# Kernel tuning notes

Hardware: AMD Instinct MI355X
Metric: run time of the kernel (lower is better)

The kernel has to match this reference:

```python
import jax, jax.numpy as jnp
import numpy as np

WS = 4      # window_size
H = 128     # hidden_size
IN = 3      # input_size (1 control + 2 state channels)
OUT = 2     # out_size = input_size - 1


def _lstm_layer(x, Wih, Whh, b):
    # x: [B, S, Din] -> ys: [B, S, H], h/c: [B, H]. PyTorch gate order i,f,g,o.
    B = x.shape[0]
    xg = jnp.einsum('bsd,gd->bsg', x, Wih) + b  # precompute input projections

    def step(carry, xt):
        h, c = carry
        g = xt + h @ Whh.T
        i, f, gg, o = jnp.split(g, 4, axis=-1)
        c = jax.nn.sigmoid(f) * c + jax.nn.sigmoid(i) * jnp.tanh(gg)
        h = jax.nn.sigmoid(o) * jnp.tanh(c)
        return (h, c), h

    z = jnp.zeros((B, Whh.shape[1]), x.dtype)
    (h, c), ys = jax.lax.scan(step, (z, z), xg.transpose(1, 0, 2))
    return ys.transpose(1, 0, 2), h, c


def _lstm2(x, p):
    (Wih0, Whh0, b0), (Wih1, Whh1, b1) = p
    y0, h0, c0 = _lstm_layer(x, Wih0, Whh0, b0)
    y1, h1, c1 = _lstm_layer(y0, Wih1, Whh1, b1)
    return y1, jnp.stack([h0, h1]), jnp.stack([c0, c1])


def _forward(traj, Wih0, Whh0, bih0, bhh0, Wih1, Whh1, bih1, bhh1, Wl, bl):
    p = ((Wih0, Whh0, bih0 + bhh0), (Wih1, Whh1, bih1 + bhh1))
    head = lambda ys: ys[:, -1] @ Wl.T + bl  # linear applied to last LSTM step (== pred[:, -1])
    T = traj.shape[1]

    # initial window on raw trajectory
    ys, h, c = _lstm2(traj[:, :WS], p)
    out = traj[:, WS - 1:WS, 1:] + head(ys)[:, None, :]  # [B, 1, OUT]

    # warm-up phase: windows mix raw traj rows with predicted rows (features ordered [ctrl, out])
    for t in range(1, WS):
        tmp = jnp.concatenate([traj[:, WS + t:WS + t + 1, 0:1], out[:, t - 1:t, :]], axis=2)
        seq = jnp.concatenate([traj[:, t:WS + t - 1, :], tmp], axis=1)  # [B, WS, IN]
        ys, h, c = _lstm2(seq, p)
        out = jnp.concatenate([out, traj[:, WS + t - 1:WS + t, 1:] + head(ys)[:, None, :]], axis=1)

    nsteps = T - 2 * WS
    idx = WS + np.arange(nsteps)[:, None] + np.arange(WS)[None, :]  # [nsteps, WS]
    ctrl = traj[:, :, 0][:, idx].transpose(1, 0, 2)[..., None]      # [nsteps, B, WS, 1]

    def step(carry, ctrl_t):
        win, _, _ = carry
        seq = jnp.concatenate([win, ctrl_t], axis=2)  # [B, WS, OUT+1]
        ys, h, c = _lstm2(seq, p)
        new = win[:, -1, :] + head(ys)                # [B, OUT]
        win = jnp.concatenate([win[:, 1:], new[:, None, :]], axis=1)
        return (win, h, c), new

    (win, h, c), news = jax.lax.scan(step, (out, h, c), ctrl)
    out = jnp.concatenate([out, news.transpose(1, 0, 2)], axis=1)  # [B, T-WS, OUT]
    return out, h, c


def setup_inputs():
    key = jax.random.key(0)
    ks = jax.random.split(key, 11)
    B, T = 128, 256
    s = 1.0 / np.sqrt(H)
    u = lambda k, shp: jax.random.uniform(k, shp, jnp.float32, -s, s)
    return dict(
        one_full_traj=jax.random.normal(ks[0], (B, T, IN), jnp.float32),
        Wih0=u(ks[1], (4 * H, IN)), Whh0=u(ks[2], (4 * H, H)),
        bih0=u(ks[3], (4 * H,)), bhh0=u(ks[4], (4 * H,)),
        Wih1=u(ks[5], (4 * H, H)), Whh1=u(ks[6], (4 * H, H)),
        bih1=u(ks[7], (4 * H,)), bhh1=u(ks[8], (4 * H,)),
        Wl=u(ks[9], (OUT, H)), bl=u(ks[10], (OUT,)),
    )


def reference(one_full_traj, Wih0, Whh0, bih0, bhh0, Wih1, Whh1, bih1, bhh1, Wl, bl):
    # returns (out, h_n, c_n) matching torch's (out, hidden)
    return _forward(one_full_traj, Wih0, Whh0, bih0, bhh0, Wih1, Whh1, bih1, bhh1, Wl, bl)
```

## Files before the change

### kernel.cpp

```cpp
#include <hip/hip_runtime.h>

typedef _Float16 half2_t __attribute__((ext_vector_type(2)));
typedef unsigned int u32;

#define NW 252

__device__ inline u32 pk(float x, float y) {
  half2_t h; h.x = (_Float16)x; h.y = (_Float16)y;
  return __builtin_bit_cast(u32, h);
}

__device__ inline float fdot2(u32 a, u32 b, float c) {
#if __has_builtin(__builtin_amdgcn_fdot2)
  return __builtin_amdgcn_fdot2(__builtin_bit_cast(half2_t, a),
                                __builtin_bit_cast(half2_t, b), c, false);
#else
  half2_t ah = __builtin_bit_cast(half2_t, a);
  half2_t bh = __builtin_bit_cast(half2_t, b);
  return c + (float)ah.x * (float)bh.x + (float)ah.y * (float)bh.y;
#endif
}

__device__ inline float fast_rcp(float x) {
#if __has_builtin(__builtin_amdgcn_rcpf)
  return __builtin_amdgcn_rcpf(x);
#else
  return 1.0f / x;
#endif
}

__device__ inline float sigf(float x)  { return fast_rcp(1.0f + __expf(-x)); }
__device__ inline float tanh_(float x) { return 1.0f - 2.0f * fast_rcp(__expf(2.0f * x) + 1.0f); }

__device__ inline float quad_reduce(float v) {
  int x = __builtin_bit_cast(int, v);
  int y = __builtin_amdgcn_update_dpp(0, x, 0xB1, 0xF, 0xF, true);
  v += __builtin_bit_cast(float, y);
  x = __builtin_bit_cast(int, v);
  y = __builtin_amdgcn_update_dpp(0, x, 0x4E, 0xF, 0xF, true);
  v += __builtin_bit_cast(float, y);
  return v;
}

#define LOAD_SLICE(dst, basehalf)                                          \
  { const uint4* _p = (const uint4*)(basehalf) + ks * 4;                   \
    uint4 _q0 = _p[0], _q1 = _p[1], _q2 = _p[2], _q3 = _p[3];              \
    dst[0]=_q0.x;  dst[1]=_q0.y;  dst[2]=_q0.z;  dst[3]=_q0.w;             \
    dst[4]=_q1.x;  dst[5]=_q1.y;  dst[6]=_q1.z;  dst[7]=_q1.w;             \
    dst[8]=_q2.x;  dst[9]=_q2.y;  dst[10]=_q2.z; dst[11]=_q2.w;            \
    dst[12]=_q3.x; dst[13]=_q3.y; dst[14]=_q3.z; dst[15]=_q3.w; }


#define L0STEP(w_, t_, p_) {                                               \
    float x0, x1, x2;                                                      \
    if ((w_) < 4) {                                                        \
      if ((w_) == 0 || (t_) < 3) {                                         \
        const float* r_ = &trajS[((w_) + (t_)) * 3];                       \
        x0 = r_[0]; x1 = r_[1]; x2 = r_[2];                                \
      } else {                        \
        x0 = trajS[(4 + (w_)) * 3];                                        \
        x1 = preds[((w_) - 1) * 2];                                        \
        x2 = preds[((w_) - 1) * 2 + 1];                                    \
      }                                                                    \
    } else {                                       \
      const int s_ = (w_) - 4;                                             \
      x0 = preds[(s_ + (t_)) * 2];                                         \
      x1 = preds[(s_ + (t_)) * 2 + 1];                                     \
      x2 = trajS[((w_) + (t_)) * 3];                                       \
    }                                                                      \
    const bool lead_ = (ks == 0);                                          \
    float a0_ = b0r[0] + w0r[0]*x0 + w0r[1] *x1 + w0r[2] *x2;              \
    float a1_ = b0r[1] + w0r[3]*x0 + w0r[4] *x1 + w0r[5] *x2;              \
    float a2_ = b0r[2] + w0r[6]*x0 + w0r[7] *x1 + w0r[8] *x2;              \
    float a3_ = b0r[3] + w0r[9]*x0 + w0r[10]*x1 + w0r[11]*x2;              \
    float acc0 = lead_ ? a0_ : 0.f, acc1 = lead_ ? a1_ : 0.f;              \
    float acc2 = lead_ ? a2_ : 0.f, acc3 = lead_ ? a3_ : 0.f;              \
    if ((t_) > 0) {                                                        \
      u32 su[16];                                                          \
      LOAD_SLICE(su, h0buf[p_]);                                           \
      _Pragma("unroll")                                                    \
      for (int kk = 0; kk < 16; ++kk) {                                    \
        acc0 = fdot2(wA[     kk], su[kk], acc0);                           \
        acc1 = fdot2(wA[16 + kk], su[kk], acc1);                           \
        acc2 = fdot2(wA[32 + kk], su[kk], acc2);                           \
        acc3 = fdot2(wA[48 + kk], su[kk], acc3);                           \
      }                                                                    \
    }                                                                      \
    acc0 = quad_reduce(acc0); acc1 = quad_reduce(acc1);                    \
    acc2 = quad_reduce(acc2); acc3 = quad_reduce(acc3);                    \
    float ig_ = sigf(acc0), fg_ = sigf(acc1);                              \
    float gg_ = tanh_(acc2), og_ = sigf(acc3);                             \
    float cp_ = (t_) ? c0 : 0.f;                                           \
    c0  = fg_ * cp_ + ig_ * gg_;                                           \
    h0f = og_ * tanh_(c0);                                                 \
    if (lead_) h0buf[(p_) ^ 1][j] = (_Float16)h0f;                         \
  }

#define L1STEP(t_, p_) {                                                   \
    const bool lead_ = (ks == 0);                                          \
    float acc0 = lead_ ? b1r[0] : 0.f, acc1 = lead_ ? b1r[1] : 0.f;        \
    float acc2 = lead_ ? b1r[2] : 0.f, acc3 = lead_ ? b1r[3] : 0.f;        \
    {                                                                      \
      u32 sy[16];                                                          \
      LOAD_SLICE(sy, h0buf[p_]);                        \
      _Pragma("unroll")                                                    \
      for (int kk = 0; kk < 16; ++kk) {                                    \
        acc0 = fdot2(wB[     kk], sy[kk], acc0);                           \
        acc1 = fdot2(wB[16 + kk], sy[kk], acc1);                           \
        acc2 = fdot2(wB[32 + kk], sy[kk], acc2);                           \
        acc3 = fdot2(wB[48 + kk], sy[kk], acc3);                           \
      }                                                                    \
    }                                                                      \
    if ((t_) > 0) {                                                        \
      u32 sh[16];                                                          \
      LOAD_SLICE(sh, h1buf[p_]);                                           \
      _Pragma("unroll")                                                    \
      for (int kk = 0; kk < 16; ++kk) {                                    \
        acc0 = fdot2(wC[     kk], sh[kk], acc0);                           \
        acc1 = fdot2(wC[16 + kk], sh[kk], acc1);                           \
        acc2 = fdot2(wC[32 + kk], sh[kk], acc2);                           \
        acc3 = fdot2(wC[48 + kk], sh[kk], acc3);                           \
      }                                                                    \
    }                                                                      \
    acc0 = quad_reduce(acc0); acc1 = quad_reduce(acc1);                    \
    acc2 = quad_reduce(acc2); acc3 = quad_reduce(acc3);                    \
    float ig_ = sigf(acc0), fg_ = sigf(acc1);                              \
    float gg_ = tanh_(acc2), og_ = sigf(acc3);                             \
    float cp_ = (t_) ? c1 : 0.f;                                           \
    c1  = fg_ * cp_ + ig_ * gg_;                                           \
    h1f = og_ * tanh_(c1);                                                 \
    if (lead_) {                                                           \
      h1buf[(p_) ^ 1][j] = (_Float16)h1f;                                  \
      if ((t_) == 3) sh_h1f[j] = h1f;           \
    }                                                                      \
  }

#define HD(w_) {                                                           \
    if (tid < 8) {                                                         \
      const int d_ = tid >> 2;                    \
      const float* wrow_ = &sh_Wl[d_ * 128 + ks * 32];                     \
      const float* hrow_ = &sh_h1f[ks * 32];                               \
      float s_ = 0.f;                                                      \
      _Pragma("unroll")                                                    \
      for (int m = 0; m < 32; ++m) s_ = fmaf(wrow_[m], hrow_[m], s_);      \
      s_ = quad_reduce(s_);                                                \
      if (ks == 0) {                                                       \
        float base_ = ((w_) < 4) ? trajS[(3 + (w_)) * 3 + 1 + d_]          \
                                 : preds[((w_) - 1) * 2 + d_];             \
        preds[(w_) * 2 + d_] = base_ + s_ + blv;                           \
      }                                                                    \
    }                                                                      \
  }

__global__ __launch_bounds__(512, 1) void lstm_roll(
    const float* __restrict__ traj,
    const float* __restrict__ Wih0, const float* __restrict__ Whh0,
    const float* __restrict__ bih0, const float* __restrict__ bhh0,
    const float* __restrict__ Wih1, const float* __restrict__ Whh1,
    const float* __restrict__ bih1, const float* __restrict__ bhh1,
    const float* __restrict__ Wl,   const float* __restrict__ bl,
    float* __restrict__ out)
{
  const int b   = blockIdx.x;
  const int B   = gridDim.x;
  const int tid = threadIdx.x;
  const int j   = tid >> 2;
  const int ks  = tid & 3;

  __shared__ __align__(16) _Float16 h0buf[2][128];
  __shared__ __align__(16) _Float16 h1buf[2][128];
  __shared__ float sh_h1f[128];
  __shared__ float sh_Wl[256];
  __shared__ float trajS[256 * 3];
  __shared__ float preds[NW * 2];

  for (int i = tid; i < 768; i += 512) trajS[i] = traj[b * 768 + i];
  if (tid < 256) sh_Wl[tid] = Wl[tid];
  float blv = 0.0f;
  if (tid < 8) blv = bl[tid >> 2];

  u32 wA[64], wB[64], wC[64];
  float b0r[4], b1r[4], w0r[12];
#pragma unroll
  for (int g = 0; g < 4; ++g) {
    const int row = g * 128 + j;
    b0r[g] = bih0[row] + bhh0[row];
    b1r[g] = bih1[row] + bhh1[row];
    w0r[g*3+0] = Wih0[row*3+0];
    w0r[g*3+1] = Wih0[row*3+1];
    w0r[g*3+2] = Wih0[row*3+2];
    const float4* pA = (const float4*)(Whh0 + row * 128 + ks * 32);
    const float4* pB = (const float4*)(Wih1 + row * 128 + ks * 32);
    const float4* pC = (const float4*)(Whh1 + row * 128 + ks * 32);
#pragma unroll
    for (int q = 0; q < 8; ++q) {
      float4 fa = pA[q], fb = pB[q], fc = pC[q];
      wA[g*16 + q*2    ] = pk(fa.x, fa.y);
      wA[g*16 + q*2 + 1] = pk(fa.z, fa.w);
      wB[g*16 + q*2    ] = pk(fb.x, fb.y);
      wB[g*16 + q*2 + 1] = pk(fb.z, fb.w);
      wC[g*16 + q*2    ] = pk(fc.x, fc.y);
      wC[g*16 + q*2 + 1] = pk(fc.z, fc.w);
    }
  }

  float c0 = 0.f, c1 = 0.f, h0f = 0.f, h1f = 0.f;

  __syncthreads();

  int p = 0;
  L0STEP(0, 0, p);
  __syncthreads(); p ^= 1;

#pragma unroll 1
  for (int w = 0; w < NW; ++w) {
    if (w > 0) HD(w - 1);
    L0STEP(w, 1, p);
    L1STEP(0, p);
    __syncthreads(); p ^= 1;
    L0STEP(w, 2, p);
    L1STEP(1, p);
    __syncthreads(); p ^= 1;
    L0STEP(w, 3, p);
    L1STEP(2, p);
    __syncthreads(); p ^= 1;
    L1STEP(3, p);
    if (w < NW - 1) L0STEP(w + 1, 0, p);
    __syncthreads(); p ^= 1;
  }

  HD(NW - 1);
  __syncthreads();

  for (int i = tid; i < NW * 2; i += 512) out[b * (NW * 2) + i] = preds[i];
  if (ks == 0) {
    const int oh = B * NW * 2;
    const int oc = oh + 2 * B * 128;
    out[oh +            b * 128 + j] = h0f;
    out[oh + B * 128 +  b * 128 + j] = h1f;
    out[oc +            b * 128 + j] = c0;
    out[oc + B * 128 +  b * 128 + j] = c1;
  }
}

extern "C" void kernel_launch(void* const* d_in, const int* in_sizes, int n_in,
                              void* d_out, int out_size, void* d_ws, size_t ws_size,
                              hipStream_t stream) {
  const float* traj = (const float*)d_in[0];
  const float* Wih0 = (const float*)d_in[1];
  const float* Whh0 = (const float*)d_in[2];
  const float* bih0 = (const float*)d_in[3];
  const float* bhh0 = (const float*)d_in[4];
  const float* Wih1 = (const float*)d_in[5];
  const float* Whh1 = (const float*)d_in[6];
  const float* bih1 = (const float*)d_in[7];
  const float* bhh1 = (const float*)d_in[8];
  const float* Wl   = (const float*)d_in[9];
  const float* bl   = (const float*)d_in[10];

  const int B = in_sizes[0] / (256 * 3);
  hipLaunchKernelGGL(lstm_roll, dim3(B), dim3(512), 0, stream,
                     traj, Wih0, Whh0, bih0, bhh0, Wih1, Whh1, bih1, bhh1,
                     Wl, bl, (float*)d_out);
}
```

Measured before the change: 1.344 ms.

## Split LSTM gates across paired lanes with 1024-thread blocks and swizzle exchange

Each hidden unit is now handled by 8 lanes instead of 4. Lanes with gh=0 compute gates i and g, lanes with gh=1 compute gates f and o, so each thread holds half the weight registers and performs half the dot products per step. The partial cell contributions are exchanged with a ds_swizzle, and the block size doubles to 1024. This shortens the per-step serial dot-product chain on the recurrent critical path, at the cost of more waves per block, an extra cross-lane exchange, and redundant transcendental evaluations.

```diff
diff --git a/kernel.cpp b/kernel.cpp
--- a/kernel.cpp
+++ b/kernel.cpp
@@ -40,6 +40,12 @@
   y = __builtin_amdgcn_update_dpp(0, x, 0x4E, 0xF, 0xF, true);
   v += __builtin_bit_cast(float, y);
   return v;
+}
+
+__device__ inline float swz4(float v) {
+  int x = __builtin_bit_cast(int, v);
+  int y = __builtin_amdgcn_ds_swizzle(x, 0x101F);
+  return __builtin_bit_cast(float, y);
 }
 
 #define LOAD_SLICE(dst, basehalf)                                          \
@@ -69,12 +75,9 @@
       x2 = trajS[((w_) + (t_)) * 3];                                       \
     }                                                                      \
     const bool lead_ = (ks == 0);                                          \
-    float a0_ = b0r[0] + w0r[0]*x0 + w0r[1] *x1 + w0r[2] *x2;              \
-    float a1_ = b0r[1] + w0r[3]*x0 + w0r[4] *x1 + w0r[5] *x2;              \
-    float a2_ = b0r[2] + w0r[6]*x0 + w0r[7] *x1 + w0r[8] *x2;              \
-    float a3_ = b0r[3] + w0r[9]*x0 + w0r[10]*x1 + w0r[11]*x2;              \
+    float a0_ = b0r[0] + w0r[0]*x0 + w0r[1]*x1 + w0r[2]*x2;                \
+    float a1_ = b0r[1] + w0r[3]*x0 + w0r[4]*x1 + w0r[5]*x2;                \
     float acc0 = lead_ ? a0_ : 0.f, acc1 = lead_ ? a1_ : 0.f;              \
-    float acc2 = lead_ ? a2_ : 0.f, acc3 = lead_ ? a3_ : 0.f;              \
     if ((t_) > 0) {                                                        \
       u32 su[16];                                                          \
       LOAD_SLICE(su, h0buf[p_]);                                           \
@@ -82,24 +85,25 @@
       for (int kk = 0; kk < 16; ++kk) {                                    \
         acc0 = fdot2(wA[     kk], su[kk], acc0);                           \
         acc1 = fdot2(wA[16 + kk], su[kk], acc1);                           \
-        acc2 = fdot2(wA[32 + kk], su[kk], acc2);                           \
-        acc3 = fdot2(wA[48 + kk], su[kk], acc3);                           \
       }                                                                    \
     }                                                                      \
     acc0 = quad_reduce(acc0); acc1 = quad_reduce(acc1);                    \
-    acc2 = quad_reduce(acc2); acc3 = quad_reduce(acc3);                    \
-    float ig_ = sigf(acc0), fg_ = sigf(acc1);                              \
-    float gg_ = tanh_(acc2), og_ = sigf(acc3);                             \
+    float sg_ = sigf(acc0);                 \
+    float tg_ = tanh_(acc1);                \
+    float og_ = sigf(acc1);                 \
+    float snd_ = gh ? sg_ : sg_ * tg_;                                     \
+    float rcv_ = swz4(snd_);                                               \
+    float A_ = gh ? rcv_ : snd_;                                           \
+    float F_ = gh ? snd_ : rcv_;                                           \
     float cp_ = (t_) ? c0 : 0.f;                                           \
-    c0  = fg_ * cp_ + ig_ * gg_;                                           \
-    h0f = og_ * tanh_(c0);                                                 \
-    if (lead_) h0buf[(p_) ^ 1][j] = (_Float16)h0f;                         \
+    c0  = F_ * cp_ + A_;                                                   \
+    h0f = og_ * tanh_(c0);                               \
+    if (lead_ && gh) h0buf[(p_) ^ 1][j] = (_Float16)h0f;                   \
   }
 
 #define L1STEP(t_, p_) {                                                   \
     const bool lead_ = (ks == 0);                                          \
     float acc0 = lead_ ? b1r[0] : 0.f, acc1 = lead_ ? b1r[1] : 0.f;        \
-    float acc2 = lead_ ? b1r[2] : 0.f, acc3 = lead_ ? b1r[3] : 0.f;        \
     {                                                                      \
       u32 sy[16];                                                          \
       LOAD_SLICE(sy, h0buf[p_]);                        \
@@ -107,8 +111,6 @@
       for (int kk = 0; kk < 16; ++kk) {                                    \
         acc0 = fdot2(wB[     kk], sy[kk], acc0);                           \
         acc1 = fdot2(wB[16 + kk], sy[kk], acc1);                           \
-        acc2 = fdot2(wB[32 + kk], sy[kk], acc2);                           \
-        acc3 = fdot2(wB[48 + kk], sy[kk], acc3);                           \
       }                                                                    \
     }                                                                      \
     if ((t_) > 0) {                                                        \
@@ -118,18 +120,20 @@
       for (int kk = 0; kk < 16; ++kk) {                                    \
         acc0 = fdot2(wC[     kk], sh[kk], acc0);                           \
         acc1 = fdot2(wC[16 + kk], sh[kk], acc1);                           \
-        acc2 = fdot2(wC[32 + kk], sh[kk], acc2);                           \
-        acc3 = fdot2(wC[48 + kk], sh[kk], acc3);                           \
       }                                                                    \
     }                                                                      \
     acc0 = quad_reduce(acc0); acc1 = quad_reduce(acc1);                    \
-    acc2 = quad_reduce(acc2); acc3 = quad_reduce(acc3);                    \
-    float ig_ = sigf(acc0), fg_ = sigf(acc1);                              \
-    float gg_ = tanh_(acc2), og_ = sigf(acc3);                             \
+    float sg_ = sigf(acc0);                                                \
+    float tg_ = tanh_(acc1);                                               \
+    float og_ = sigf(acc1);                                                \
+    float snd_ = gh ? sg_ : sg_ * tg_;                                     \
+    float rcv_ = swz4(snd_);                                               \
+    float A_ = gh ? rcv_ : snd_;                                           \
+    float F_ = gh ? snd_ : rcv_;                                           \
     float cp_ = (t_) ? c1 : 0.f;                                           \
-    c1  = fg_ * cp_ + ig_ * gg_;                                           \
-    h1f = og_ * tanh_(c1);                                                 \
-    if (lead_) {                                                           \
+    c1  = F_ * cp_ + A_;                                                   \
+    h1f = og_ * tanh_(c1);                               \
+    if (lead_ && gh) {                                                     \
       h1buf[(p_) ^ 1][j] = (_Float16)h1f;                                  \
       if ((t_) == 3) sh_h1f[j] = h1f;           \
     }                                                                      \
@@ -152,7 +156,7 @@
     }                                                                      \
   }
 
-__global__ __launch_bounds__(512, 1) void lstm_roll(
+__global__ __launch_bounds__(1024, 1) void lstm_roll(
     const float* __restrict__ traj,
     const float* __restrict__ Wih0, const float* __restrict__ Whh0,
     const float* __restrict__ bih0, const float* __restrict__ bhh0,
@@ -164,8 +168,9 @@
   const int b   = blockIdx.x;
   const int B   = gridDim.x;
   const int tid = threadIdx.x;
-  const int j   = tid >> 2;
   const int ks  = tid & 3;
+  const int gh  = (tid >> 2) & 1;
+  const int j   = tid >> 3;
 
   __shared__ __align__(16) _Float16 h0buf[2][128];
   __shared__ __align__(16) _Float16 h1buf[2][128];
@@ -174,33 +179,33 @@
   __shared__ float trajS[256 * 3];
   __shared__ float preds[NW * 2];
 
-  for (int i = tid; i < 768; i += 512) trajS[i] = traj[b * 768 + i];
+  for (int i = tid; i < 768; i += 1024) trajS[i] = traj[b * 768 + i];
   if (tid < 256) sh_Wl[tid] = Wl[tid];
   float blv = 0.0f;
   if (tid < 8) blv = bl[tid >> 2];
 
-  u32 wA[64], wB[64], wC[64];
-  float b0r[4], b1r[4], w0r[12];
+  u32 wA[32], wB[32], wC[32];
+  float b0r[2], b1r[2], w0r[6];
 #pragma unroll
-  for (int g = 0; g < 4; ++g) {
-    const int row = g * 128 + j;
-    b0r[g] = bih0[row] + bhh0[row];
-    b1r[g] = bih1[row] + bhh1[row];
-    w0r[g*3+0] = Wih0[row*3+0];
-    w0r[g*3+1] = Wih0[row*3+1];
-    w0r[g*3+2] = Wih0[row*3+2];
+  for (int g2 = 0; g2 < 2; ++g2) {
+    const int row = (gh + 2 * g2) * 128 + j;
+    b0r[g2] = bih0[row] + bhh0[row];
+    b1r[g2] = bih1[row] + bhh1[row];
+    w0r[g2*3+0] = Wih0[row*3+0];
+    w0r[g2*3+1] = Wih0[row*3+1];
+    w0r[g2*3+2] = Wih0[row*3+2];
     const float4* pA = (const float4*)(Whh0 + row * 128 + ks * 32);
     const float4* pB = (const float4*)(Wih1 + row * 128 + ks * 32);
     const float4* pC = (const float4*)(Whh1 + row * 128 + ks * 32);
 #pragma unroll
     for (int q = 0; q < 8; ++q) {
       float4 fa = pA[q], fb = pB[q], fc = pC[q];
-      wA[g*16 + q*2    ] = pk(fa.x, fa.y);
-      wA[g*16 + q*2 + 1] = pk(fa.z, fa.w);
-      wB[g*16 + q*2    ] = pk(fb.x, fb.y);
-      wB[g*16 + q*2 + 1] = pk(fb.z, fb.w);
-      wC[g*16 + q*2    ] = pk(fc.x, fc.y);
-      wC[g*16 + q*2 + 1] = pk(fc.z, fc.w);
+      wA[g2*16 + q*2    ] = pk(fa.x, fa.y);
+      wA[g2*16 + q*2 + 1] = pk(fa.z, fa.w);
+      wB[g2*16 + q*2    ] = pk(fb.x, fb.y);
+      wB[g2*16 + q*2 + 1] = pk(fb.z, fb.w);
+      wC[g2*16 + q*2    ] = pk(fc.x, fc.y);
+      wC[g2*16 + q*2 + 1] = pk(fc.z, fc.w);
     }
   }
 
@@ -232,8 +237,8 @@
   HD(NW - 1);
   __syncthreads();
 
-  for (int i = tid; i < NW * 2; i += 512) out[b * (NW * 2) + i] = preds[i];
-  if (ks == 0) {
+  for (int i = tid; i < NW * 2; i += 1024) out[b * (NW * 2) + i] = preds[i];
+  if (ks == 0 && gh == 1) {
     const int oh = B * NW * 2;
     const int oc = oh + 2 * B * 128;
     out[oh +            b * 128 + j] = h0f;
@@ -259,7 +264,7 @@
   const float* bl   = (const float*)d_in[10];
 
   const int B = in_sizes[0] / (256 * 3);
-  hipLaunchKernelGGL(lstm_roll, dim3(B), dim3(512), 0, stream,
+  hipLaunchKernelGGL(lstm_roll, dim3(B), dim3(1024), 0, stream,
                      traj, Wih0, Whh0, bih0, bhh0, Wih1, Whh1, bih1, bhh1,
                      Wl, bl, (float*)d_out);
 }
```

Measured after the change: 1.927 ms. 43.4% more time.

## Move LSTM weights out of registers into LDS and a prepacked global buffer

Applied to the files above, without the earlier changes.

The before kernel kept all three fp16-packed 128x512 weight slices (Whh0, Wih1, Whh1) in registers, 192 u32 per thread. Now only Whh0 stays in registers. Whh1 is packed into a 128 KB LDS array, and Wih1 is prepacked by a separate kernel into a global workspace that is read through cache on every step. Layer-0 input weights and biases also move to LDS. This lowers register pressure, which may avoid spills or allow higher occupancy, but adds per-step LDS and global loads to the serial recurrence, plus an extra kernel launch.

```diff
diff --git a/kernel.cpp b/kernel.cpp
--- a/kernel.cpp
+++ b/kernel.cpp
@@ -42,14 +42,42 @@
   return v;
 }
 
-#define LOAD_SLICE(dst, basehalf)                                          \
-  { const uint4* _p = (const uint4*)(basehalf) + ks * 4;                   \
-    uint4 _q0 = _p[0], _q1 = _p[1], _q2 = _p[2], _q3 = _p[3];              \
-    dst[0]=_q0.x;  dst[1]=_q0.y;  dst[2]=_q0.z;  dst[3]=_q0.w;             \
-    dst[4]=_q1.x;  dst[5]=_q1.y;  dst[6]=_q1.z;  dst[7]=_q1.w;             \
-    dst[8]=_q2.x;  dst[9]=_q2.y;  dst[10]=_q2.z; dst[11]=_q2.w;            \
-    dst[12]=_q3.x; dst[13]=_q3.y; dst[14]=_q3.z; dst[15]=_q3.w; }
-
+__device__ inline uint4 pk8(const float* p) {
+  const float4* s = (const float4*)p;
+  float4 a = s[0], b = s[1];
+  return make_uint4(pk(a.x, a.y), pk(a.z, a.w), pk(b.x, b.y), pk(b.z, b.w));
+}
+
+#define DOTQ(sq, g0_, g1_, g2_, g3_) {                                     \
+    acc0 = fdot2(g0_.x, sq.x, acc0); acc0 = fdot2(g0_.y, sq.y, acc0);      \
+    acc0 = fdot2(g0_.z, sq.z, acc0); acc0 = fdot2(g0_.w, sq.w, acc0);      \
+    acc1 = fdot2(g1_.x, sq.x, acc1); acc1 = fdot2(g1_.y, sq.y, acc1);      \
+    acc1 = fdot2(g1_.z, sq.z, acc1); acc1 = fdot2(g1_.w, sq.w, acc1);      \
+    acc2 = fdot2(g2_.x, sq.x, acc2); acc2 = fdot2(g2_.y, sq.y, acc2);      \
+    acc2 = fdot2(g2_.z, sq.z, acc2); acc2 = fdot2(g2_.w, sq.w, acc2);      \
+    acc3 = fdot2(g3_.x, sq.x, acc3); acc3 = fdot2(g3_.y, sq.y, acc3);      \
+    acc3 = fdot2(g3_.z, sq.z, acc3); acc3 = fdot2(g3_.w, sq.w, acc3); }
+
+
+#define WBCHUNK(kq_, sq_) {                                                \
+    uint4 g0_, g1_, g2_, g3_;                                              \
+    if constexpr (WSMODE) {                                                \
+      g0_ = ws[(0*4+(kq_))*512 + tid]; g1_ = ws[(1*4+(kq_))*512 + tid];    \
+      g2_ = ws[(2*4+(kq_))*512 + tid]; g3_ = ws[(3*4+(kq_))*512 + tid];    \
+    } else {                                                               \
+      g0_ = pk8(Wih1 + (0*128+j)*128 + ks*32 + (kq_)*8);                   \
+      g1_ = pk8(Wih1 + (1*128+j)*128 + ks*32 + (kq_)*8);                   \
+      g2_ = pk8(Wih1 + (2*128+j)*128 + ks*32 + (kq_)*8);                   \
+      g3_ = pk8(Wih1 + (3*128+j)*128 + ks*32 + (kq_)*8);                   \
+    }                                                                      \
+    DOTQ(sq_, g0_, g1_, g2_, g3_); }
+
+#define WCCHUNK(kq_, sq_) {                                                \
+    uint4 e0_ = wCl[(0*4+(kq_))*512 + tid];                                \
+    uint4 e1_ = wCl[(1*4+(kq_))*512 + tid];                                \
+    uint4 e2_ = wCl[(2*4+(kq_))*512 + tid];                                \
+    uint4 e3_ = wCl[(3*4+(kq_))*512 + tid];                                \
+    DOTQ(sq_, e0_, e1_, e2_, e3_); }
 
 #define L0STEP(w_, t_, p_) {                                               \
     float x0, x1, x2;                                                      \
@@ -68,23 +96,22 @@
       x1 = preds[(s_ + (t_)) * 2 + 1];                                     \
       x2 = trajS[((w_) + (t_)) * 3];                                       \
     }                                                                      \
-    const bool lead_ = (ks == 0);                                          \
-    float a0_ = b0r[0] + w0r[0]*x0 + w0r[1] *x1 + w0r[2] *x2;              \
-    float a1_ = b0r[1] + w0r[3]*x0 + w0r[4] *x1 + w0r[5] *x2;              \
-    float a2_ = b0r[2] + w0r[6]*x0 + w0r[7] *x1 + w0r[8] *x2;              \
-    float a3_ = b0r[3] + w0r[9]*x0 + w0r[10]*x1 + w0r[11]*x2;              \
-    float acc0 = lead_ ? a0_ : 0.f, acc1 = lead_ ? a1_ : 0.f;              \
-    float acc2 = lead_ ? a2_ : 0.f, acc3 = lead_ ? a3_ : 0.f;              \
+    float acc0 = 0.f, acc1 = 0.f, acc2 = 0.f, acc3 = 0.f;                  \
+    if (ks == 0) {                          \
+      float4 q0_ = ldsG0[j*4+0], q1_ = ldsG0[j*4+1];                       \
+      float4 q2_ = ldsG0[j*4+2], q3_ = ldsG0[j*4+3];                       \
+      acc0 = q0_.w + q0_.x*x0 + q0_.y*x1 + q0_.z*x2;                       \
+      acc1 = q1_.w + q1_.x*x0 + q1_.y*x1 + q1_.z*x2;                       \
+      acc2 = q2_.w + q2_.x*x0 + q2_.y*x1 + q2_.z*x2;                       \
+      acc3 = q3_.w + q3_.x*x0 + q3_.y*x1 + q3_.z*x2;                       \
+    }                                                                      \
     if ((t_) > 0) {                                                        \
-      u32 su[16];                                                          \
-      LOAD_SLICE(su, h0buf[p_]);                                           \
-      _Pragma("unroll")                                                    \
-      for (int kk = 0; kk < 16; ++kk) {                                    \
-        acc0 = fdot2(wA[     kk], su[kk], acc0);                           \
-        acc1 = fdot2(wA[16 + kk], su[kk], acc1);                           \
-        acc2 = fdot2(wA[32 + kk], su[kk], acc2);                           \
-        acc3 = fdot2(wA[48 + kk], su[kk], acc3);                           \
-      }                                                                    \
+      const uint4* hb_ = (const uint4*)(h0buf[p_]) + ks*4;                 \
+      uint4 s0_ = hb_[0], s1_ = hb_[1], s2_ = hb_[2], s3_ = hb_[3];        \
+      DOTQ(s0_, A0q0, A1q0, A2q0, A3q0);                                   \
+      DOTQ(s1_, A0q1, A1q1, A2q1, A3q1);                                   \
+      DOTQ(s2_, A0q2, A1q2, A2q2, A3q2);                                   \
+      DOTQ(s3_, A0q3, A1q3, A2q3, A3q3);                                   \
     }                                                                      \
     acc0 = quad_reduce(acc0); acc1 = quad_reduce(acc1);                    \
     acc2 = quad_reduce(acc2); acc3 = quad_reduce(acc3);                    \
@@ -93,34 +120,24 @@
     float cp_ = (t_) ? c0 : 0.f;                                           \
     c0  = fg_ * cp_ + ig_ * gg_;                                           \
     h0f = og_ * tanh_(c0);                                                 \
-    if (lead_) h0buf[(p_) ^ 1][j] = (_Float16)h0f;                         \
+    if (ks == 0) h0buf[(p_) ^ 1][j] = (_Float16)h0f;                       \
   }
 
 #define L1STEP(t_, p_) {                                                   \
-    const bool lead_ = (ks == 0);                                          \
-    float acc0 = lead_ ? b1r[0] : 0.f, acc1 = lead_ ? b1r[1] : 0.f;        \
-    float acc2 = lead_ ? b1r[2] : 0.f, acc3 = lead_ ? b1r[3] : 0.f;        \
+    float acc0 = 0.f, acc1 = 0.f, acc2 = 0.f, acc3 = 0.f;                  \
+    if (ks == 0) { float4 bv_ = ldsB1[j];                                  \
+      acc0 = bv_.x; acc1 = bv_.y; acc2 = bv_.z; acc3 = bv_.w; }            \
     {                                                                      \
-      u32 sy[16];                                                          \
-      LOAD_SLICE(sy, h0buf[p_]);                        \
-      _Pragma("unroll")                                                    \
-      for (int kk = 0; kk < 16; ++kk) {                                    \
-        acc0 = fdot2(wB[     kk], sy[kk], acc0);                           \
-        acc1 = fdot2(wB[16 + kk], sy[kk], acc1);                           \
-        acc2 = fdot2(wB[32 + kk], sy[kk], acc2);                           \
-        acc3 = fdot2(wB[48 + kk], sy[kk], acc3);                           \
-      }                                                                    \
+      const uint4* hb_ = (const uint4*)(h0buf[p_]) + ks*4;                 \
+      uint4 s0_ = hb_[0], s1_ = hb_[1], s2_ = hb_[2], s3_ = hb_[3];        \
+      WBCHUNK(0, s0_); WBCHUNK(1, s1_);                                    \
+      WBCHUNK(2, s2_); WBCHUNK(3, s3_);                                    \
     }                                                                      \
     if ((t_) > 0) {                                                        \
-      u32 sh[16];                                                          \
-      LOAD_SLICE(sh, h1buf[p_]);                                           \
-      _Pragma("unroll")                                                    \
-      for (int kk = 0; kk < 16; ++kk) {                                    \
-        acc0 = fdot2(wC[     kk], sh[kk], acc0);                           \
-        acc1 = fdot2(wC[16 + kk], sh[kk], acc1);                           \
-        acc2 = fdot2(wC[32 + kk], sh[kk], acc2);                           \
-        acc3 = fdot2(wC[48 + kk], sh[kk], acc3);                           \
-      }                                                                    \
+      const uint4* hc_ = (const uint4*)(h1buf[p_]) + ks*4;                 \
+      uint4 r0_ = hc_[0], r1_ = hc_[1], r2_ = hc_[2], r3_ = hc_[3];        \
+      WCCHUNK(0, r0_); WCCHUNK(1, r1_);                                    \
+      WCCHUNK(2, r2_); WCCHUNK(3, r3_);                                    \
     }                                                                      \
     acc0 = quad_reduce(acc0); acc1 = quad_reduce(acc1);                    \
     acc2 = quad_reduce(acc2); acc3 = quad_reduce(acc3);                    \
@@ -129,7 +146,7 @@
     float cp_ = (t_) ? c1 : 0.f;                                           \
     c1  = fg_ * cp_ + ig_ * gg_;                                           \
     h1f = og_ * tanh_(c1);                                                 \
-    if (lead_) {                                                           \
+    if (ks == 0) {                                                         \
       h1buf[(p_) ^ 1][j] = (_Float16)h1f;                                  \
       if ((t_) == 3) sh_h1f[j] = h1f;           \
     }                                                                      \
@@ -152,13 +169,23 @@
     }                                                                      \
   }
 
-__global__ __launch_bounds__(512, 1) void lstm_roll(
+__global__ void wb_prepack(const float* __restrict__ Wih1, uint4* __restrict__ ws) {
+  const int e = blockIdx.x * blockDim.x + threadIdx.x;
+  if (e >= 8192) return;
+  const int t = e & 511, q = e >> 9;
+  const int g = q >> 2, kq = q & 3, j = t >> 2, ks = t & 3;
+  ws[e] = pk8(Wih1 + (g * 128 + j) * 128 + ks * 32 + kq * 8);
+}
+
+template <int WSMODE>
+__global__ __launch_bounds__(512) void lstm_roll(
     const float* __restrict__ traj,
     const float* __restrict__ Wih0, const float* __restrict__ Whh0,
     const float* __restrict__ bih0, const float* __restrict__ bhh0,
     const float* __restrict__ Wih1, const float* __restrict__ Whh1,
     const float* __restrict__ bih1, const float* __restrict__ bhh1,
     const float* __restrict__ Wl,   const float* __restrict__ bl,
+    const uint4* __restrict__ ws,
     float* __restrict__ out)
 {
   const int b   = blockIdx.x;
@@ -173,36 +200,51 @@
   __shared__ float sh_Wl[256];
   __shared__ float trajS[256 * 3];
   __shared__ float preds[NW * 2];
+  __shared__ float4 ldsG0[512];
+  __shared__ float4 ldsB1[128];
+  __shared__ uint4  wCl[8192];
 
   for (int i = tid; i < 768; i += 512) trajS[i] = traj[b * 768 + i];
   if (tid < 256) sh_Wl[tid] = Wl[tid];
   float blv = 0.0f;
   if (tid < 8) blv = bl[tid >> 2];
 
-  u32 wA[64], wB[64], wC[64];
-  float b0r[4], b1r[4], w0r[12];
+  if (tid < 128) {
+    const int jj = tid;
 #pragma unroll
-  for (int g = 0; g < 4; ++g) {
-    const int row = g * 128 + j;
-    b0r[g] = bih0[row] + bhh0[row];
-    b1r[g] = bih1[row] + bhh1[row];
-    w0r[g*3+0] = Wih0[row*3+0];
-    w0r[g*3+1] = Wih0[row*3+1];
-    w0r[g*3+2] = Wih0[row*3+2];
-    const float4* pA = (const float4*)(Whh0 + row * 128 + ks * 32);
-    const float4* pB = (const float4*)(Wih1 + row * 128 + ks * 32);
-    const float4* pC = (const float4*)(Whh1 + row * 128 + ks * 32);
+    for (int g = 0; g < 4; ++g) {
+      const int row = g * 128 + jj;
+      ldsG0[jj * 4 + g] = make_float4(Wih0[row * 3 + 0], Wih0[row * 3 + 1],
+                                      Wih0[row * 3 + 2], bih0[row] + bhh0[row]);
+    }
+    ldsB1[jj] = make_float4(bih1[0 * 128 + jj] + bhh1[0 * 128 + jj],
+                            bih1[1 * 128 + jj] + bhh1[1 * 128 + jj],
+                            bih1[2 * 128 + jj] + bhh1[2 * 128 + jj],
+                            bih1[3 * 128 + jj] + bhh1[3 * 128 + jj]);
+  }
+
 #pragma unroll
-    for (int q = 0; q < 8; ++q) {
-      float4 fa = pA[q], fb = pB[q], fc = pC[q];
-      wA[g*16 + q*2    ] = pk(fa.x, fa.y);
-      wA[g*16 + q*2 + 1] = pk(fa.z, fa.w);
-      wB[g*16 + q*2    ] = pk(fb.x, fb.y);
-      wB[g*16 + q*2 + 1] = pk(fb.z, fb.w);
-      wC[g*16 + q*2    ] = pk(fc.x, fc.y);
-      wC[g*16 + q*2 + 1] = pk(fc.z, fc.w);
-    }
-  }
+  for (int q = 0; q < 16; ++q) {
+    const int g = q >> 2, kq = q & 3;
+    wCl[q * 512 + tid] = pk8(Whh1 + (g * 128 + j) * 128 + ks * 32 + kq * 8);
+  }
+
+  uint4 A0q0 = pk8(Whh0 + (0*128+j)*128 + ks*32 + 0*8);
+  uint4 A0q1 = pk8(Whh0 + (0*128+j)*128 + ks*32 + 1*8);
+  uint4 A0q2 = pk8(Whh0 + (0*128+j)*128 + ks*32 + 2*8);
+  uint4 A0q3 = pk8(Whh0 + (0*128+j)*128 + ks*32 + 3*8);
+  uint4 A1q0 = pk8(Whh0 + (1*128+j)*128 + ks*32 + 0*8);
+  uint4 A1q1 = pk8(Whh0 + (1*128+j)*128 + ks*32 + 1*8);
+  uint4 A1q2 = pk8(Whh0 + (1*128+j)*128 + ks*32 + 2*8);
+  uint4 A1q3 = pk8(Whh0 + (1*128+j)*128 + ks*32 + 3*8);
+  uint4 A2q0 = pk8(Whh0 + (2*128+j)*128 + ks*32 + 0*8);
+  uint4 A2q1 = pk8(Whh0 + (2*128+j)*128 + ks*32 + 1*8);
+  uint4 A2q2 = pk8(Whh0 + (2*128+j)*128 + ks*32 + 2*8);
+  uint4 A2q3 = pk8(Whh0 + (2*128+j)*128 + ks*32 + 3*8);
+  uint4 A3q0 = pk8(Whh0 + (3*128+j)*128 + ks*32 + 0*8);
+  uint4 A3q1 = pk8(Whh0 + (3*128+j)*128 + ks*32 + 1*8);
+  uint4 A3q2 = pk8(Whh0 + (3*128+j)*128 + ks*32 + 2*8);
+  uint4 A3q3 = pk8(Whh0 + (3*128+j)*128 + ks*32 + 3*8);
 
   float c0 = 0.f, c1 = 0.f, h0f = 0.f, h1f = 0.f;
 
@@ -259,7 +301,16 @@
   const float* bl   = (const float*)d_in[10];
 
   const int B = in_sizes[0] / (256 * 3);
-  hipLaunchKernelGGL(lstm_roll, dim3(B), dim3(512), 0, stream,
-                     traj, Wih0, Whh0, bih0, bhh0, Wih1, Whh1, bih1, bhh1,
-                     Wl, bl, (float*)d_out);
-}
+
+  if (d_ws != nullptr && ws_size >= 8192 * sizeof(uint4)) {
+    hipLaunchKernelGGL(wb_prepack, dim3(16), dim3(512), 0, stream,
+                       Wih1, (uint4*)d_ws);
+    hipLaunchKernelGGL((lstm_roll<1>), dim3(B), dim3(512), 0, stream,
+                       traj, Wih0, Whh0, bih0, bhh0, Wih1, Whh1, bih1, bhh1,
+                       Wl, bl, (const uint4*)d_ws, (float*)d_out);
+  } else {
+    hipLaunchKernelGGL((lstm_roll<0>), dim3(B), dim3(512), 0, stream,
+                       traj, Wih0, Whh0, bih0, bhh0, Wih1, Whh1, bih1, bhh1,
+                       Wl, bl, (const uint4*)nullptr, (float*)d_out);
+  }
+}
```

After: 1.433 ms. 1.07x slower.
